# Kernel optimization log

Measured on AMD Instinct MI355X. Metric: run time of the kernel, lower is better.

The kernel has to match this reference:

```python
import jax, jax.numpy as jnp
import numpy as np

VOCAB = 5000; EMB = 300; AUDIO = 74; HID = 128
D1 = 16; D2 = 16; DIM = D1 * D2
UNITS = 128; CELL = 64; OUT = 1
B = 32; S = 32
NGRAMS = (1, 3)


def _lstm(x, w_ih, w_hh, b_ih, b_hh):
    # PyTorch LSTMCell semantics, gate order i, f, g, o
    Bb = x.shape[0]; H = w_hh.shape[1]
    def step(carry, xt):
        h, c = carry
        gates = xt @ w_ih.T + h @ w_hh.T + b_ih + b_hh
        i, f, g, o = jnp.split(gates, 4, axis=-1)
        c = jax.nn.sigmoid(f) * c + jax.nn.sigmoid(i) * jnp.tanh(g)
        h = jax.nn.sigmoid(o) * jnp.tanh(c)
        return (h, c), h
    init = (jnp.zeros((Bb, H), x.dtype), jnp.zeros((Bb, H), x.dtype))
    _, hs = jax.lax.scan(step, init, jnp.swapaxes(x, 0, 1))
    return jnp.swapaxes(hs, 0, 1)  # (B, S, H)


def _windows(x, n):
    # zero-padded n-gram windows: (B, S, d) -> (B, S, n, d)
    xp = jnp.pad(x, ((0, 0), (0, n - 1), (0, 0)))
    s = x.shape[1]
    return jnp.stack([xp[:, k:k + s, :] for k in range(n)], axis=2)


def setup_inputs() -> dict:
    key = jax.random.key(0)
    ks = jax.random.split(key, 26)
    g = lambda i, shape, sc=0.05: jax.random.normal(ks[i], shape, dtype=jnp.float32) * sc
    return dict(
        word_indexes=jax.random.randint(ks[0], (B, S), 0, VOCAB),
        audio=jax.random.normal(ks[1], (B, S, AUDIO), dtype=jnp.float32),
        lookup_table=g(2, (VOCAB, EMB), 0.5),
        phase_tab0=g(3, (VOCAB, D1), 3.14),
        phase_tab1=g(4, (VOCAB, D2), 3.14),
        w_ih=g(5, (4 * HID, EMB)), w_hh=g(6, (4 * HID, HID)),
        b_ih=g(7, (4 * HID,)), b_hh=g(8, (4 * HID,)),
        w_lin=g(9, (D1, HID)), b_lin=g(10, (D1,)),
        w1=g(11, (D2, AUDIO)), b1=g(12, (D2,)),
        w2=g(13, (D2, D2)), b2=g(14, (D2,)),
        w3=g(15, (D2, D2)), b3=g(16, (D2,)),
        modality_weights=jnp.zeros((2,), jnp.float32),
        meas_r=g(17, (UNITS, DIM), 0.5), meas_i=g(18, (UNITS, DIM), 0.5),
        fw1=g(19, (CELL, UNITS)), fb1=g(20, (CELL,)),
        fw2=g(21, (CELL, CELL)), fb2=g(22, (CELL,)),
        fw3=g(23, (OUT, CELL)), fb3=jnp.zeros((OUT,), jnp.float32),
    )


def reference(word_indexes, audio, lookup_table, phase_tab0, phase_tab1,
              w_ih, w_hh, b_ih, b_hh, w_lin, b_lin,
              w1, b1, w2, b2, w3, b3,
              modality_weights, meas_r, meas_i,
              fw1, fb1, fw2, fb2, fw3, fb3):
    eps = 1e-10
    # amplitude subnets (dropout rates are 0 / eval mode)
    text = lookup_table[word_indexes]                      # (B,S,EMB)
    h = _lstm(text, w_ih, w_hh, b_ih, b_hh)
    amp0 = h @ w_lin.T + b_lin                             # (B,S,D1)
    a = jax.nn.relu(audio @ w1.T + b1)
    a = jax.nn.relu(a @ w2.T + b2)
    amp1 = jax.nn.relu(a @ w3.T + b3)                      # (B,S,D2)
    ph0 = phase_tab0[word_indexes]
    ph1 = phase_tab1[word_indexes]

    def branch(amp, ph):
        norm = jnp.linalg.norm(amp, axis=-1, keepdims=True)
        ampn = amp / (norm + eps)
        return norm, ampn * jnp.cos(ph), ampn * jnp.sin(ph)

    n0, r0, i0 = branch(amp0, ph0)
    n1, r1, i1 = branch(amp1, ph1)
    mw = jax.nn.softmax(modality_weights)
    weight = mw[0] * n0 + mw[1] * n1                       # (B,S,1)

    # sequential complex tensor product across modalities,
    # starting from (real=1, imag=1) as in the original code
    tpr = r0 - i0
    tpi = r0 + i0
    real = jnp.einsum('bsi,bsj->bsij', tpr, r1) - jnp.einsum('bsi,bsj->bsij', tpi, i1)
    imag = jnp.einsum('bsi,bsj->bsij', tpr, i1) + jnp.einsum('bsi,bsj->bsij', tpi, r1)
    real = real.reshape(B, S, DIM)
    imag = imag.reshape(B, S, DIM)

    # measurement kernel: unit-norm complex vectors
    kn = jnp.sqrt(jnp.sum(meas_r ** 2 + meas_i ** 2, axis=-1, keepdims=True)) + eps
    vr = meas_r / kn
    vi = meas_i / kn

    probs = []
    for n in NGRAMS:
        wr = _windows(real, n)                             # (B,S,n,DIM)
        wi = _windows(imag, n)
        ww = jax.nn.softmax(_windows(weight, n)[..., 0], axis=-1)  # (B,S,n)
        # complex mixture: rho = sum_n w_n |v_n><v_n|
        rho_r = (jnp.einsum('bsn,bsni,bsnj->bsij', ww, wr, wr)
                 + jnp.einsum('bsn,bsni,bsnj->bsij', ww, wi, wi))
        rho_i = (jnp.einsum('bsn,bsni,bsnj->bsij', ww, wi, wr)
                 - jnp.einsum('bsn,bsni,bsnj->bsij', ww, wr, wi))
        # measurement: Re(v^H rho v) per unit
        m = (jnp.einsum('bsij,ui,uj->bsu', rho_r, vr, vr)
             + jnp.einsum('bsij,ui,uj->bsu', rho_r, vi, vi)
             + jnp.einsum('bsij,ui,uj->bsu', rho_i, vi, vr)
             - jnp.einsum('bsij,ui,uj->bsu', rho_i, vr, vi))
        probs.append(m)
    probs = jnp.concatenate(probs, axis=1)                 # (B, S*len(NGRAMS), UNITS)
    feat = jnp.max(probs, axis=1)                          # 'max' pooling
    y = jax.nn.relu(feat @ fw1.T + fb1)
    y = jax.nn.relu(y @ fw2.T + fb2)
    return y @ fw3.T + fb3                                 # (B, OUT)
```

## Files before the change

### kernel.cpp

```cpp
#include <hip/hip_runtime.h>
#include <math.h>


static constexpr unsigned XW0_OFF  = 0u;
static constexpr unsigned XW1_OFF  = 524288u;
static constexpr unsigned HOUT_OFF = 1048576u;
static constexpr unsigned XMAT_OFF = HOUT_OFF + 131072u;
static constexpr unsigned WT_OFF   = XMAT_OFF + 524288u;
static constexpr unsigned VPP_OFF  = WT_OFF + 1024u;
static constexpr unsigned PP_OFF   = VPP_OFF + 131072u;
static constexpr unsigned PP_HALF  = 262144u;

__global__ __launch_bounds__(256) void k1_xw_gemm(
    const int* __restrict__ widx, const float* __restrict__ lut,
    const float* __restrict__ w_ih, const float* __restrict__ b_ih,
    const float* __restrict__ b_hh,
    const float* __restrict__ mr, const float* __restrict__ mi,
    float* __restrict__ ws)
{
  const int bid = blockIdx.x;
  const int t = threadIdx.x;

  if (bid >= 256) {
    const int u = bid - 256;
    float r  = mr[u * 256 + t];
    float ii = mi[u * 256 + t];
    float sq = r * r + ii * ii;
    #pragma unroll
    for (int off = 1; off < 64; off <<= 1) sq += __shfl_xor(sq, off);
    __shared__ float wsum[4];
    if ((t & 63) == 0) wsum[t >> 6] = sq;
    __syncthreads();
    float tot = wsum[0] + wsum[1] + wsum[2] + wsum[3];
    float inv = 1.0f / (sqrtf(tot) + 1e-10f);
    float vr = r * inv, vi = ii * inv;
    float* vpp = ws + VPP_OFF;
    vpp[(2 * u) * 512 + t]           = vr;
    vpp[(2 * u) * 512 + 256 + t]     = vi;
    vpp[(2 * u + 1) * 512 + t]       = -vi;
    vpp[(2 * u + 1) * 512 + 256 + t] = vr;
    return;
  }

  const int rb = bid & 15, cb = (bid >> 4) & 7, kq = bid >> 7;
  const int R = rb * 64, C = cb * 64;
  const int kbase_g = kq * 152;
  const int ktot = kq ? 148 : 152;

  __shared__ alignas(16) float As[32][68];
  __shared__ alignas(16) float Ws[32][68];

  float acc[4][4] = {};
  const int r0 = (t & 15) * 4, j0 = (t >> 4) * 4;

  for (int kt = 0; kt < 5; ++kt) {
    int kl = ktot - kt * 32; if (kl > 32) kl = 32;
    #pragma unroll
    for (int pass = 0; pass < 2; ++pass) {
      int rr = (t >> 3) + pass * 32;
      int kk4 = (t & 7) * 4;
      float4 av = make_float4(0.f, 0.f, 0.f, 0.f);
      float4 wv = make_float4(0.f, 0.f, 0.f, 0.f);
      if (kk4 < kl) {
        int gk = kbase_g + kt * 32 + kk4;
        int word = widx[R + rr];
        av = *(const float4*)&lut[word * 300 + gk];
        wv = *(const float4*)&w_ih[(C + rr) * 300 + gk];
      }
      As[kk4 + 0][rr] = av.x; As[kk4 + 1][rr] = av.y;
      As[kk4 + 2][rr] = av.z; As[kk4 + 3][rr] = av.w;
      Ws[kk4 + 0][rr] = wv.x; Ws[kk4 + 1][rr] = wv.y;
      Ws[kk4 + 2][rr] = wv.z; Ws[kk4 + 3][rr] = wv.w;
    }
    __syncthreads();
    #pragma unroll
    for (int k = 0; k < 32; ++k) {
      float4 a4 = *(const float4*)&As[k][r0];
      float4 w4 = *(const float4*)&Ws[k][j0];
      float ar[4] = {a4.x, a4.y, a4.z, a4.w};
      float wr[4] = {w4.x, w4.y, w4.z, w4.w};
      #pragma unroll
      for (int i2 = 0; i2 < 4; ++i2)
        #pragma unroll
        for (int j2 = 0; j2 < 4; ++j2)
          acc[i2][j2] = fmaf(ar[i2], wr[j2], acc[i2][j2]);
    }
    __syncthreads();
  }

  float* xw = ws + (kq ? XW1_OFF : XW0_OFF);
  #pragma unroll
  for (int i2 = 0; i2 < 4; ++i2) {
    int row = R + r0 + i2, col = C + j0;
    float4 v = make_float4(acc[i2][0], acc[i2][1], acc[i2][2], acc[i2][3]);
    if (kq == 0) {
      v.x += b_ih[col + 0] + b_hh[col + 0];
      v.y += b_ih[col + 1] + b_hh[col + 1];
      v.z += b_ih[col + 2] + b_hh[col + 2];
      v.w += b_ih[col + 3] + b_hh[col + 3];
    }
    *(float4*)&xw[row * 512 + col] = v;
  }
}

__global__ __launch_bounds__(512, 2) void k2_lstm(
    const float* __restrict__ w_hh, float* __restrict__ ws)
{
  const int b = blockIdx.x;
  const int t = threadIdx.x;
  const int jj = t >> 2;
  const int kq = t & 3;

  float4 wreg[4][8];
  #pragma unroll
  for (int g = 0; g < 4; ++g) {
    const float* wp = w_hh + (jj + 128 * g) * 128 + kq * 32;
    #pragma unroll
    for (int i = 0; i < 8; ++i) wreg[g][i] = *(const float4*)&wp[i * 4];
  }

  __shared__ alignas(16) float hbuf[2][128];
  if (t < 128) hbuf[0][t] = 0.f;

  const float* xw0 = ws + XW0_OFF;
  const float* xw1 = ws + XW1_OFF;
  float* hout = ws + HOUT_OFF;

  float c = 0.f;
  float hhist[32];
  __syncthreads();

  for (int s = 0; s < 32; ++s) {
    const int bs = b * 32 + s;
    float xg0 = 0.f, xg1 = 0.f, xg2 = 0.f, xg3 = 0.f;
    if (kq == 0) {
      int base = bs * 512 + jj;
      xg0 = xw0[base +   0] + xw1[base +   0];
      xg1 = xw0[base + 128] + xw1[base + 128];
      xg2 = xw0[base + 256] + xw1[base + 256];
      xg3 = xw0[base + 384] + xw1[base + 384];
    }
    const float4* hb = (const float4*)hbuf[s & 1] + kq * 8;
    float a0 = 0.f, a1 = 0.f, a2 = 0.f, a3 = 0.f;
    #pragma unroll
    for (int i = 0; i < 8; ++i) {
      float4 h4 = hb[i];
      a0 = fmaf(wreg[0][i].x, h4.x, fmaf(wreg[0][i].y, h4.y, fmaf(wreg[0][i].z, h4.z, fmaf(wreg[0][i].w, h4.w, a0))));
      a1 = fmaf(wreg[1][i].x, h4.x, fmaf(wreg[1][i].y, h4.y, fmaf(wreg[1][i].z, h4.z, fmaf(wreg[1][i].w, h4.w, a1))));
      a2 = fmaf(wreg[2][i].x, h4.x, fmaf(wreg[2][i].y, h4.y, fmaf(wreg[2][i].z, h4.z, fmaf(wreg[2][i].w, h4.w, a2))));
      a3 = fmaf(wreg[3][i].x, h4.x, fmaf(wreg[3][i].y, h4.y, fmaf(wreg[3][i].z, h4.z, fmaf(wreg[3][i].w, h4.w, a3))));
    }
    a0 += __shfl_xor(a0, 1); a0 += __shfl_xor(a0, 2);
    a1 += __shfl_xor(a1, 1); a1 += __shfl_xor(a1, 2);
    a2 += __shfl_xor(a2, 1); a2 += __shfl_xor(a2, 2);
    a3 += __shfl_xor(a3, 1); a3 += __shfl_xor(a3, 2);
    if (kq == 0) {
      float gi = xg0 + a0, gf = xg1 + a1, gg = xg2 + a2, go = xg3 + a3;
      float si = 1.f / (1.f + __expf(-gi));
      float sf = 1.f / (1.f + __expf(-gf));
      float tg = 1.f - 2.f / (1.f + __expf(2.f * gg));
      float so = 1.f / (1.f + __expf(-go));
      c = sf * c + si * tg;
      float tc = 1.f - 2.f / (1.f + __expf(2.f * c));
      float hn = so * tc;
      hbuf[(s + 1) & 1][jj] = hn;
      hhist[s] = hn;
    }
    __syncthreads();
  }
  if (kq == 0) {
    #pragma unroll
    for (int s = 0; s < 32; ++s) hout[(b * 32 + s) * 128 + jj] = hhist[s];
  }
}

__global__ __launch_bounds__(256) void k3_mix(
    const int* __restrict__ widx, const float* __restrict__ audio,
    const float* __restrict__ ph0t, const float* __restrict__ ph1t,
    const float* __restrict__ w_lin, const float* __restrict__ b_lin,
    const float* __restrict__ w1, const float* __restrict__ b1,
    const float* __restrict__ w2, const float* __restrict__ b2,
    const float* __restrict__ w3, const float* __restrict__ b3,
    const float* __restrict__ modw, float* __restrict__ ws)
{
  const int bs = blockIdx.x;
  const int t = threadIdx.x;
  __shared__ float amp0[16], a1s[16], a2s[16], amp1[16];
  __shared__ float tpr[16], tpi[16], r1s[16], i1s[16];
  __shared__ float nn[2];

  const float* hrow = ws + HOUT_OFF + bs * 128;
  if (t < 16) {
    float acc = b_lin[t];
    for (int u = 0; u < 128; ++u) acc = fmaf(hrow[u], w_lin[t * 128 + u], acc);
    amp0[t] = acc;
  } else if (t >= 64 && t < 80) {
    int d = t - 64;
    float acc = b1[d];
    for (int k = 0; k < 74; ++k) acc = fmaf(audio[bs * 74 + k], w1[d * 74 + k], acc);
    a1s[d] = fmaxf(acc, 0.f);
  }
  __syncthreads();
  if (t < 16) {
    float acc = b2[t];
    #pragma unroll
    for (int k = 0; k < 16; ++k) acc = fmaf(a1s[k], w2[t * 16 + k], acc);
    a2s[t] = fmaxf(acc, 0.f);
  }
  __syncthreads();
  if (t < 16) {
    float acc = b3[t];
    #pragma unroll
    for (int k = 0; k < 16; ++k) acc = fmaf(a2s[k], w3[t * 16 + k], acc);
    amp1[t] = fmaxf(acc, 0.f);
  }
  __syncthreads();
  if (t == 0) {
    float sq = 0.f;
    #pragma unroll
    for (int d = 0; d < 16; ++d) sq += amp0[d] * amp0[d];
    nn[0] = sqrtf(sq);
  } else if (t == 64) {
    float sq = 0.f;
    #pragma unroll
    for (int d = 0; d < 16; ++d) sq += amp1[d] * amp1[d];
    nn[1] = sqrtf(sq);
  }
  __syncthreads();
  const int word = widx[bs];
  if (t < 16) {
    float k0 = amp0[t] / (nn[0] + 1e-10f);
    float ph = ph0t[word * 16 + t];
    float cc = cosf(ph), ssn = sinf(ph);
    tpr[t] = k0 * (cc - ssn);
    tpi[t] = k0 * (cc + ssn);
  } else if (t >= 64 && t < 80) {
    int d = t - 64;
    float k1 = amp1[d] / (nn[1] + 1e-10f);
    float ph = ph1t[word * 16 + d];
    r1s[d] = k1 * cosf(ph);
    i1s[d] = k1 * sinf(ph);
  } else if (t == 128) {
    float e0 = __expf(modw[0]), e1 = __expf(modw[1]);
    float mw0 = e0 / (e0 + e1);
    ws[WT_OFF + bs] = mw0 * nn[0] + (1.f - mw0) * nn[1];
  }
  __syncthreads();
  const int i2 = t >> 4, j2 = t & 15;
  float rr = tpr[i2] * r1s[j2] - tpi[i2] * i1s[j2];
  float im = tpr[i2] * i1s[j2] + tpi[i2] * r1s[j2];
  float* X = ws + XMAT_OFF;
  X[bs * 512 + t] = rr;
  X[bs * 512 + 256 + t] = im;
}

__global__ __launch_bounds__(256) void k4_meas(float* __restrict__ ws)
{
  const int bid = blockIdx.x, t = threadIdx.x;
  const int rb = bid & 15, cb = (bid >> 4) & 3, kq = bid >> 6;
  const int R = rb * 64, C = cb * 64;
  const float* X = ws + XMAT_OFF;
  const float* V = ws + VPP_OFF;
  __shared__ alignas(16) float Xs[32][68];
  __shared__ alignas(16) float Vs[32][68];
  float acc[4][4] = {};
  const int r0 = (t & 15) * 4, j0 = (t >> 4) * 4;

  for (int kt = 0; kt < 4; ++kt) {
    #pragma unroll
    for (int pass = 0; pass < 2; ++pass) {
      int rr = (t >> 3) + pass * 32;
      int kk4 = (t & 7) * 4;
      int gk = kq * 128 + kt * 32 + kk4;
      float4 xv = *(const float4*)&X[(R + rr) * 512 + gk];
      float4 vv = *(const float4*)&V[(C + rr) * 512 + gk];
      Xs[kk4 + 0][rr] = xv.x; Xs[kk4 + 1][rr] = xv.y;
      Xs[kk4 + 2][rr] = xv.z; Xs[kk4 + 3][rr] = xv.w;
      Vs[kk4 + 0][rr] = vv.x; Vs[kk4 + 1][rr] = vv.y;
      Vs[kk4 + 2][rr] = vv.z; Vs[kk4 + 3][rr] = vv.w;
    }
    __syncthreads();
    #pragma unroll
    for (int k = 0; k < 32; ++k) {
      float4 a4 = *(const float4*)&Xs[k][r0];
      float4 w4 = *(const float4*)&Vs[k][j0];
      float ar[4] = {a4.x, a4.y, a4.z, a4.w};
      float wr[4] = {w4.x, w4.y, w4.z, w4.w};
      #pragma unroll
      for (int i2 = 0; i2 < 4; ++i2)
        #pragma unroll
        for (int j2 = 0; j2 < 4; ++j2)
          acc[i2][j2] = fmaf(ar[i2], wr[j2], acc[i2][j2]);
    }
    __syncthreads();
  }
  float* Pp = ws + PP_OFF + (unsigned)kq * PP_HALF;
  #pragma unroll
  for (int i2 = 0; i2 < 4; ++i2) {
    float4 v = make_float4(acc[i2][0], acc[i2][1], acc[i2][2], acc[i2][3]);
    *(float4*)&Pp[(R + r0 + i2) * 256 + C + j0] = v;
  }
}

__global__ __launch_bounds__(128) void k5_final(
    const float* __restrict__ fw1, const float* __restrict__ fb1,
    const float* __restrict__ fw2, const float* __restrict__ fb2,
    const float* __restrict__ fw3, const float* __restrict__ fb3,
    const float* __restrict__ ws, float* __restrict__ out)
{
  const int b = blockIdx.x, t = threadIdx.x;
  __shared__ float ewt[34], feat[128], y1[64], y2[64];
  if (t < 32) ewt[t] = expf(ws[WT_OFF + b * 32 + t]);
  if (t == 0) { ewt[32] = 1.f; ewt[33] = 1.f; }
  __syncthreads();

  const float* Pp = ws + PP_OFF;
  float p[32];
  #pragma unroll
  for (int s = 0; s < 32; ++s) {
    int bs = b * 32 + s;
    float A = 0.f, Bv = 0.f;
    #pragma unroll
    for (int kq = 0; kq < 4; ++kq) {
      A  += Pp[kq * PP_HALF + bs * 256 + 2 * t];
      Bv += Pp[kq * PP_HALF + bs * 256 + 2 * t + 1];
    }
    p[s] = A * A + Bv * Bv;
  }
  float m = -1e30f;
  #pragma unroll
  for (int s = 0; s < 32; ++s) m = fmaxf(m, p[s]);
  #pragma unroll
  for (int s = 0; s < 32; ++s) {
    float e0 = ewt[s], e1 = ewt[s + 1], e2 = ewt[s + 2];
    float num = e0 * p[s];
    if (s + 1 < 32) num += e1 * p[s + 1];
    if (s + 2 < 32) num += e2 * p[s + 2];
    m = fmaxf(m, num / (e0 + e1 + e2));
  }
  feat[t] = m;
  __syncthreads();
  if (t < 64) {
    float acc = fb1[t];
    for (int k = 0; k < 128; ++k) acc = fmaf(feat[k], fw1[t * 128 + k], acc);
    y1[t] = fmaxf(acc, 0.f);
  }
  __syncthreads();
  if (t < 64) {
    float acc = fb2[t];
    #pragma unroll
    for (int k = 0; k < 64; ++k) acc = fmaf(y1[k], fw2[t * 64 + k], acc);
    y2[t] = fmaxf(acc, 0.f);
  }
  __syncthreads();
  if (t == 0) {
    float acc = fb3[0];
    #pragma unroll
    for (int k = 0; k < 64; ++k) acc = fmaf(y2[k], fw3[k], acc);
    out[b] = acc;
  }
}

extern "C" void kernel_launch(void* const* d_in, const int* in_sizes, int n_in,
                              void* d_out, int out_size, void* d_ws, size_t ws_size,
                              hipStream_t stream) {
  const int*   widx  = (const int*)d_in[0];
  const float* audio = (const float*)d_in[1];
  const float* lut   = (const float*)d_in[2];
  const float* ph0   = (const float*)d_in[3];
  const float* ph1   = (const float*)d_in[4];
  const float* w_ih  = (const float*)d_in[5];
  const float* w_hh  = (const float*)d_in[6];
  const float* b_ih  = (const float*)d_in[7];
  const float* b_hh  = (const float*)d_in[8];
  const float* w_lin = (const float*)d_in[9];
  const float* b_lin = (const float*)d_in[10];
  const float* w1    = (const float*)d_in[11];
  const float* b1    = (const float*)d_in[12];
  const float* w2    = (const float*)d_in[13];
  const float* b2    = (const float*)d_in[14];
  const float* w3    = (const float*)d_in[15];
  const float* b3    = (const float*)d_in[16];
  const float* modw  = (const float*)d_in[17];
  const float* mr    = (const float*)d_in[18];
  const float* mi    = (const float*)d_in[19];
  const float* fw1   = (const float*)d_in[20];
  const float* fb1   = (const float*)d_in[21];
  const float* fw2   = (const float*)d_in[22];
  const float* fb2   = (const float*)d_in[23];
  const float* fw3   = (const float*)d_in[24];
  const float* fb3   = (const float*)d_in[25];
  float* ws  = (float*)d_ws;
  float* out = (float*)d_out;

  k1_xw_gemm<<<dim3(384), dim3(256), 0, stream>>>(widx, lut, w_ih, b_ih, b_hh, mr, mi, ws);
  k2_lstm<<<dim3(32), dim3(512), 0, stream>>>(w_hh, ws);
  k3_mix<<<dim3(1024), dim3(256), 0, stream>>>(widx, audio, ph0, ph1, w_lin, b_lin,
                                               w1, b1, w2, b2, w3, b3, modw, ws);
  k4_meas<<<dim3(256), dim3(256), 0, stream>>>(ws);
  k5_final<<<dim3(32), dim3(128), 0, stream>>>(fw1, fb1, fw2, fb2, fw3, fb3, ws, out);
}
```

Baseline: 198.3 us.

## Split LSTM recurrence across 8 lanes per unit and preload input gates

The LSTM kernel now uses 1024 threads per block, with 8 lanes per hidden unit each covering a 16-element slice of the hidden vector. Each thread holds the full W_hh slice in registers and preloads its precomputed input-gate terms before the time loop, so no global loads sit on the serial path. The shared-memory reads of the hidden state are rotated per lane group to avoid bank conflicts, and the gate activations are computed redundantly by every lane so there is no branch. The final kernel spreads the pooling over 512 threads through shared memory, at the cost of extra synchronisation and register pressure.

```diff
diff --git a/kernel.cpp b/kernel.cpp
--- a/kernel.cpp
+++ b/kernel.cpp
@@ -103,74 +103,84 @@
   }
 }
 
-__global__ __launch_bounds__(512, 2) void k2_lstm(
+__global__ __launch_bounds__(1024, 4) void k2_lstm(
     const float* __restrict__ w_hh, float* __restrict__ ws)
 {
   const int b = blockIdx.x;
   const int t = threadIdx.x;
-  const int jj = t >> 2;
-  const int kq = t & 3;
-
-  float4 wreg[4][8];
+  const int jj = t >> 3;
+  const int ko = t & 7;
+  const int gstar = ko & 3;
+  const int shalf = ko >> 2;
+  const int rot = (ko >> 1) & 3;
+
+  float4 wreg[4][4];
   #pragma unroll
   for (int g = 0; g < 4; ++g) {
-    const float* wp = w_hh + (jj + 128 * g) * 128 + kq * 32;
-    #pragma unroll
-    for (int i = 0; i < 8; ++i) wreg[g][i] = *(const float4*)&wp[i * 4];
-  }
+    const float* wp = w_hh + (g * 128 + jj) * 128 + ko * 16;
+    #pragma unroll
+    for (int cc = 0; cc < 4; ++cc) {
+      int ci = (cc + rot) & 3;
+      wreg[g][cc] = *(const float4*)&wp[ci * 4];
+    }
+  }
+
+  const float* xw0 = ws + XW0_OFF;
+  const float* xw1 = ws + XW1_OFF;
+  float xg[16];
+  {
+    const int base = (b * 32 + shalf * 16) * 512 + gstar * 128 + jj;
+    #pragma unroll
+    for (int i = 0; i < 16; ++i)
+      xg[i] = xw0[base + i * 512] + xw1[base + i * 512];
+  }
+  const float m0 = (gstar == 0) ? 1.f : 0.f;
+  const float m1 = (gstar == 1) ? 1.f : 0.f;
+  const float m2 = (gstar == 2) ? 1.f : 0.f;
+  const float m3 = (gstar == 3) ? 1.f : 0.f;
 
   __shared__ alignas(16) float hbuf[2][128];
   if (t < 128) hbuf[0][t] = 0.f;
-
-  const float* xw0 = ws + XW0_OFF;
-  const float* xw1 = ws + XW1_OFF;
   float* hout = ws + HOUT_OFF;
-
   float c = 0.f;
-  float hhist[32];
-  __syncthreads();
-
+  __syncthreads();
+
+  #pragma unroll
   for (int s = 0; s < 32; ++s) {
-    const int bs = b * 32 + s;
-    float xg0 = 0.f, xg1 = 0.f, xg2 = 0.f, xg3 = 0.f;
-    if (kq == 0) {
-      int base = bs * 512 + jj;
-      xg0 = xw0[base +   0] + xw1[base +   0];
-      xg1 = xw0[base + 128] + xw1[base + 128];
-      xg2 = xw0[base + 256] + xw1[base + 256];
-      xg3 = xw0[base + 384] + xw1[base + 384];
-    }
-    const float4* hb = (const float4*)hbuf[s & 1] + kq * 8;
+    const float* hb = hbuf[s & 1] + ko * 16;
     float a0 = 0.f, a1 = 0.f, a2 = 0.f, a3 = 0.f;
     #pragma unroll
-    for (int i = 0; i < 8; ++i) {
-      float4 h4 = hb[i];
-      a0 = fmaf(wreg[0][i].x, h4.x, fmaf(wreg[0][i].y, h4.y, fmaf(wreg[0][i].z, h4.z, fmaf(wreg[0][i].w, h4.w, a0))));
-      a1 = fmaf(wreg[1][i].x, h4.x, fmaf(wreg[1][i].y, h4.y, fmaf(wreg[1][i].z, h4.z, fmaf(wreg[1][i].w, h4.w, a1))));
-      a2 = fmaf(wreg[2][i].x, h4.x, fmaf(wreg[2][i].y, h4.y, fmaf(wreg[2][i].z, h4.z, fmaf(wreg[2][i].w, h4.w, a2))));
-      a3 = fmaf(wreg[3][i].x, h4.x, fmaf(wreg[3][i].y, h4.y, fmaf(wreg[3][i].z, h4.z, fmaf(wreg[3][i].w, h4.w, a3))));
-    }
-    a0 += __shfl_xor(a0, 1); a0 += __shfl_xor(a0, 2);
-    a1 += __shfl_xor(a1, 1); a1 += __shfl_xor(a1, 2);
-    a2 += __shfl_xor(a2, 1); a2 += __shfl_xor(a2, 2);
-    a3 += __shfl_xor(a3, 1); a3 += __shfl_xor(a3, 2);
-    if (kq == 0) {
-      float gi = xg0 + a0, gf = xg1 + a1, gg = xg2 + a2, go = xg3 + a3;
-      float si = 1.f / (1.f + __expf(-gi));
-      float sf = 1.f / (1.f + __expf(-gf));
-      float tg = 1.f - 2.f / (1.f + __expf(2.f * gg));
-      float so = 1.f / (1.f + __expf(-go));
-      c = sf * c + si * tg;
-      float tc = 1.f - 2.f / (1.f + __expf(2.f * c));
-      float hn = so * tc;
+    for (int cc = 0; cc < 4; ++cc) {
+      int ci = (cc + rot) & 3;
+      float4 h4 = *(const float4*)&hb[ci * 4];
+      a0 = fmaf(wreg[0][cc].x, h4.x, fmaf(wreg[0][cc].y, h4.y, fmaf(wreg[0][cc].z, h4.z, fmaf(wreg[0][cc].w, h4.w, a0))));
+      a1 = fmaf(wreg[1][cc].x, h4.x, fmaf(wreg[1][cc].y, h4.y, fmaf(wreg[1][cc].z, h4.z, fmaf(wreg[1][cc].w, h4.w, a1))));
+      a2 = fmaf(wreg[2][cc].x, h4.x, fmaf(wreg[2][cc].y, h4.y, fmaf(wreg[2][cc].z, h4.z, fmaf(wreg[2][cc].w, h4.w, a2))));
+      a3 = fmaf(wreg[3][cc].x, h4.x, fmaf(wreg[3][cc].y, h4.y, fmaf(wreg[3][cc].z, h4.z, fmaf(wreg[3][cc].w, h4.w, a3))));
+    }
+    {
+      float xv = ((s >> 4) == shalf) ? xg[s & 15] : 0.f;
+      a0 = fmaf(xv, m0, a0);
+      a1 = fmaf(xv, m1, a1);
+      a2 = fmaf(xv, m2, a2);
+      a3 = fmaf(xv, m3, a3);
+    }
+    a0 += __shfl_xor(a0, 1); a0 += __shfl_xor(a0, 2); a0 += __shfl_xor(a0, 4);
+    a1 += __shfl_xor(a1, 1); a1 += __shfl_xor(a1, 2); a1 += __shfl_xor(a1, 4);
+    a2 += __shfl_xor(a2, 1); a2 += __shfl_xor(a2, 2); a2 += __shfl_xor(a2, 4);
+    a3 += __shfl_xor(a3, 1); a3 += __shfl_xor(a3, 2); a3 += __shfl_xor(a3, 4);
+    float si = 1.f / (1.f + __expf(-a0));
+    float sf = 1.f / (1.f + __expf(-a1));
+    float tg = 1.f - 2.f / (1.f + __expf(2.f * a2));
+    float so = 1.f / (1.f + __expf(-a3));
+    c = sf * c + si * tg;
+    float tc = 1.f - 2.f / (1.f + __expf(2.f * c));
+    float hn = so * tc;
+    if (ko == 0) {
       hbuf[(s + 1) & 1][jj] = hn;
-      hhist[s] = hn;
-    }
-    __syncthreads();
-  }
-  if (kq == 0) {
-    #pragma unroll
-    for (int s = 0; s < 32; ++s) hout[(b * 32 + s) * 128 + jj] = hhist[s];
+      hout[(b * 32 + s) * 128 + jj] = hn;
+    }
+    __syncthreads();
   }
 }
 
@@ -302,43 +312,53 @@
   }
 }
 
-__global__ __launch_bounds__(128) void k5_final(
+__global__ __launch_bounds__(512) void k5_final(
     const float* __restrict__ fw1, const float* __restrict__ fb1,
     const float* __restrict__ fw2, const float* __restrict__ fb2,
     const float* __restrict__ fw3, const float* __restrict__ fb3,
     const float* __restrict__ ws, float* __restrict__ out)
 {
   const int b = blockIdx.x, t = threadIdx.x;
-  __shared__ float ewt[34], feat[128], y1[64], y2[64];
-  if (t < 32) ewt[t] = expf(ws[WT_OFF + b * 32 + t]);
-  if (t == 0) { ewt[32] = 1.f; ewt[33] = 1.f; }
+  const int u = t & 127, sg = t >> 7;
+  __shared__ float ewt[34];
+  __shared__ float pl[32][128];
+  __shared__ float fred[4][128];
+  __shared__ float feat[128], y1[64], y2[64];
+  if (t < 32) ewt[t] = __expf(ws[WT_OFF + b * 32 + t]);
+  if (t >= 32 && t < 34) ewt[t] = 1.f;
   __syncthreads();
 
   const float* Pp = ws + PP_OFF;
-  float p[32];
-  #pragma unroll
-  for (int s = 0; s < 32; ++s) {
+  #pragma unroll
+  for (int i = 0; i < 8; ++i) {
+    int s = sg * 8 + i;
     int bs = b * 32 + s;
     float A = 0.f, Bv = 0.f;
     #pragma unroll
     for (int kq = 0; kq < 4; ++kq) {
-      A  += Pp[kq * PP_HALF + bs * 256 + 2 * t];
-      Bv += Pp[kq * PP_HALF + bs * 256 + 2 * t + 1];
-    }
-    p[s] = A * A + Bv * Bv;
-  }
+      A  += Pp[kq * PP_HALF + bs * 256 + 2 * u];
+      Bv += Pp[kq * PP_HALF + bs * 256 + 2 * u + 1];
+    }
+    pl[s][u] = A * A + Bv * Bv;
+  }
+  __syncthreads();
+
   float m = -1e30f;
   #pragma unroll
-  for (int s = 0; s < 32; ++s) m = fmaxf(m, p[s]);
-  #pragma unroll
-  for (int s = 0; s < 32; ++s) {
+  for (int i = 0; i < 8; ++i) {
+    int s = sg * 8 + i;
+    float p0 = pl[s][u];
+    m = fmaxf(m, p0);
     float e0 = ewt[s], e1 = ewt[s + 1], e2 = ewt[s + 2];
-    float num = e0 * p[s];
-    if (s + 1 < 32) num += e1 * p[s + 1];
-    if (s + 2 < 32) num += e2 * p[s + 2];
+    float num = e0 * p0;
+    if (s + 1 < 32) num += e1 * pl[s + 1][u];
+    if (s + 2 < 32) num += e2 * pl[s + 2][u];
     m = fmaxf(m, num / (e0 + e1 + e2));
   }
-  feat[t] = m;
+  fred[sg][u] = m;
+  __syncthreads();
+  if (t < 128)
+    feat[t] = fmaxf(fmaxf(fred[0][t], fred[1][t]), fmaxf(fred[2][t], fred[3][t]));
   __syncthreads();
   if (t < 64) {
     float acc = fb1[t];
@@ -394,9 +414,9 @@
   float* out = (float*)d_out;
 
   k1_xw_gemm<<<dim3(384), dim3(256), 0, stream>>>(widx, lut, w_ih, b_ih, b_hh, mr, mi, ws);
-  k2_lstm<<<dim3(32), dim3(512), 0, stream>>>(w_hh, ws);
+  k2_lstm<<<dim3(32), dim3(1024), 0, stream>>>(w_hh, ws);
   k3_mix<<<dim3(1024), dim3(256), 0, stream>>>(widx, audio, ph0, ph1, w_lin, b_lin,
                                                w1, b1, w2, b2, w3, b3, modw, ws);
   k4_meas<<<dim3(256), dim3(256), 0, stream>>>(ws);
-  k5_final<<<dim3(32), dim3(128), 0, stream>>>(fw1, fb1, fw2, fb2, fw3, fb3, ws, out);
-}
+  k5_final<<<dim3(32), dim3(512), 0, stream>>>(fw1, fb1, fw2, fb2, fw3, fb3, ws, out);
+}
```

Result: faster. 194.1 us (-2.1%).
